# Kernel tuning notes

Measured on AMD Instinct MI355X. Metric: run time of the kernel, lower is better.

The kernel has to match this reference:

```python
import jax, jax.numpy as jnp
import numpy as np

N_NODES = 100_000
N_EDGES = 3_200_000
HIDDEN = 16


def setup_inputs() -> dict:
    key = jax.random.key(0)
    k1, k2, k3, k4 = jax.random.split(key, 4)
    x = jax.random.normal(k1, (N_NODES, 3), dtype=jnp.float32)
    edge_index = jax.random.randint(k2, (2, N_EDGES), 0, N_NODES, dtype=jnp.int32)
    # Glorot-style init for the two GCN layers (PyG GCNConv: lin weight + bias)
    W1 = jax.random.normal(k3, (3, HIDDEN), dtype=jnp.float32) * (1.0 / np.sqrt(3.0))
    b1 = jnp.zeros((HIDDEN,), dtype=jnp.float32)
    W2 = jax.random.normal(k4, (HIDDEN, 1), dtype=jnp.float32) * (1.0 / np.sqrt(HIDDEN))
    b2 = jnp.zeros((1,), dtype=jnp.float32)
    return {"x": x, "edge_index": edge_index, "W1": W1, "b1": b1, "W2": W2, "b2": b2}


def reference(x, edge_index, W1, b1, W2, b2):
    n = x.shape[0]  # static under jit
    # GCNConv default: add self-loops, symmetric degree normalization
    self_loop = jnp.arange(n, dtype=edge_index.dtype)
    src = jnp.concatenate([edge_index[0], self_loop])
    dst = jnp.concatenate([edge_index[1], self_loop])
    deg = jax.ops.segment_sum(jnp.ones_like(src, dtype=x.dtype), dst, num_segments=n)
    inv_sqrt_deg = jnp.where(deg > 0, jax.lax.rsqrt(jnp.maximum(deg, 1.0)), 0.0)
    norm = inv_sqrt_deg[src] * inv_sqrt_deg[dst]  # [E+N]

    def gcn_conv(h, W, b):
        h = h @ W  # linear transform first (cheaper: small out dim)
        msg = norm[:, None] * h[src]  # gather + scale
        return jax.ops.segment_sum(msg, dst, num_segments=n) + b  # scatter-add

    h = jax.nn.relu(gcn_conv(x, W1, b1))
    out = gcn_conv(h, W2, b2)
    return out.squeeze(-1)  # [N]
```

## Files before the change

kernel.cpp:

```cpp
#include <hip/hip_runtime.h>

#define HIDDEN 16
#define FB 128
#define FB_SHIFT 7
#define NBK_MAX 4096
#define FCHUNK 4096
#define FTH 512
#define STH 512
#define NXCD 8
#define CB 1024
#define CB_SHIFT 10
#define NCB_MAX 512
#define CHUNK 4096
#define SPL 8
#define BT 1024

__device__ __forceinline__ int xcd_chunk(int bid, int nwg) {
    if (nwg < NXCD) return bid;
    int q = nwg / NXCD, r = nwg % NXCD;
    int x = bid % NXCD, k = bid / NXCD;
    return (x < r ? x * (q + 1) : r * (q + 1) + (x - r) * q) + k;
}


__global__ __launch_bounds__(FTH) void
k_histf(const int* __restrict__ dst, int e, int nbk, int nchunk,
        unsigned int* __restrict__ hcT) {
    __shared__ unsigned int h[NBK_MAX];
    for (int i = threadIdx.x; i < nbk; i += FTH) h[i] = 0u;
    __syncthreads();
    int c = xcd_chunk(blockIdx.x, nchunk);
    int start = c * FCHUNK;
    int end = min(start + FCHUNK, e);
    if (end - start == FCHUNK) {
        int i = start + threadIdx.x;
#pragma unroll
        for (int k = 0; k < FCHUNK / FTH; k++, i += FTH)
            atomicAdd(&h[((unsigned)dst[i]) >> FB_SHIFT], 1u);
    } else {
        for (int i = start + threadIdx.x; i < end; i += FTH)
            atomicAdd(&h[((unsigned)dst[i]) >> FB_SHIFT], 1u);
    }
    __syncthreads();
    for (int j = threadIdx.x; j < nbk; j += FTH)
        hcT[(size_t)j * nchunk + c] = h[j];
}

__global__ void k_scanf(unsigned int* __restrict__ hcT,
                        unsigned int* __restrict__ cntc, int nchunk) {
    __shared__ unsigned int ps[256];
    __shared__ unsigned int carry;
    int b = blockIdx.x, t = threadIdx.x;
    if (t == 0) carry = 0u;
    __syncthreads();
    size_t row = (size_t)b * nchunk;
    for (int t0 = 0; t0 < nchunk; t0 += 1024) {
        int i0 = t0 + t * 4;
        unsigned v0 = 0, v1 = 0, v2 = 0, v3 = 0;
        if (i0 + 3 < nchunk) {
            v0 = hcT[row + i0];     v1 = hcT[row + i0 + 1];
            v2 = hcT[row + i0 + 2]; v3 = hcT[row + i0 + 3];
        } else {
            if (i0     < nchunk) v0 = hcT[row + i0];
            if (i0 + 1 < nchunk) v1 = hcT[row + i0 + 1];
            if (i0 + 2 < nchunk) v2 = hcT[row + i0 + 2];
            if (i0 + 3 < nchunk) v3 = hcT[row + i0 + 3];
        }
        unsigned s1v = v0 + v1, s2v = s1v + v2, s3v = s2v + v3;
        ps[t] = s3v;
        __syncthreads();
        for (int off = 1; off < 256; off <<= 1) {
            unsigned u = (t >= off) ? ps[t - off] : 0u;
            __syncthreads();
            ps[t] += u;
            __syncthreads();
        }
        unsigned base = carry + ps[t] - s3v;
        if (i0     < nchunk) hcT[row + i0]     = base;
        if (i0 + 1 < nchunk) hcT[row + i0 + 1] = base + v0;
        if (i0 + 2 < nchunk) hcT[row + i0 + 2] = base + s1v;
        if (i0 + 3 < nchunk) hcT[row + i0 + 3] = base + s2v;
        __syncthreads();
        if (t == 255) carry += ps[255];
        __syncthreads();
    }
    if (t == 0) cntc[b] = carry;
}

__global__ __launch_bounds__(1024) void
k_scanb(const unsigned int* __restrict__ cntc, int nbk,
        unsigned int* __restrict__ basec,
        unsigned int* __restrict__ rowptr, int n, unsigned int e) {
    __shared__ unsigned int tsum[1024];
    int t = threadIdx.x;
    int K = (nbk + 1023) / 1024;
    unsigned int s = 0;
    for (int k = 0; k < K; k++) {
        int i = t * K + k;
        if (i < nbk) s += cntc[i];
    }
    tsum[t] = s;
    __syncthreads();
    for (int off = 1; off < 1024; off <<= 1) {
        unsigned int v = (t >= off) ? tsum[t - off] : 0u;
        __syncthreads();
        tsum[t] += v;
        __syncthreads();
    }
    unsigned int run = (t == 0) ? 0u : tsum[t - 1];
    for (int k = 0; k < K; k++) {
        int i = t * K + k;
        if (i < nbk) { basec[i] = run; run += cntc[i]; }
    }
    if (t == 1023) basec[nbk] = tsum[1023];
    if (t == 0) rowptr[n] = e;
}

__global__ __launch_bounds__(FTH) void
k_fillf(const int* __restrict__ src, const int* __restrict__ dst,
        int e, int nbk, int nchunk,
        const unsigned int* __restrict__ basec,
        const unsigned int* __restrict__ hcT,
        unsigned int* __restrict__ tmp) {
    __shared__ unsigned int h[NBK_MAX];
    __shared__ unsigned int lb[NBK_MAX];
    int c = xcd_chunk(blockIdx.x, nchunk);
    for (int j = threadIdx.x; j < nbk; j += FTH) {
        lb[j] = basec[j] + hcT[(size_t)j * nchunk + c];
        h[j] = 0u;
    }
    __syncthreads();
    int start = c * FCHUNK;
    int end = min(start + FCHUNK, e);
    if (end - start == FCHUNK) {
        int i = start + threadIdx.x;
#pragma unroll
        for (int k = 0; k < FCHUNK / FTH; k++, i += FTH) {
            unsigned int d = (unsigned)dst[i];
            unsigned int s = (unsigned)src[i];
            unsigned int b = d >> FB_SHIFT;
            unsigned int r = atomicAdd(&h[b], 1u);
            tmp[lb[b] + r] = (s << FB_SHIFT) | (d & (FB - 1u));
        }
    } else {
        for (int i = start + threadIdx.x; i < end; i += FTH) {
            unsigned int d = (unsigned)dst[i];
            unsigned int s = (unsigned)src[i];
            unsigned int b = d >> FB_SHIFT;
            unsigned int r = atomicAdd(&h[b], 1u);
            tmp[lb[b] + r] = (s << FB_SHIFT) | (d & (FB - 1u));
        }
    }
}

__global__ __launch_bounds__(STH) void
k_sortN(const unsigned int* __restrict__ tmp,
        const unsigned int* __restrict__ basec,
        const float* __restrict__ x,
        unsigned int* __restrict__ rowptr, unsigned int* __restrict__ tmp2,
        float4* __restrict__ xs4, int n) {
    __shared__ unsigned int cnt[FB];
    __shared__ unsigned int sc[FB];
    __shared__ unsigned int cur[FB];
    int t = threadIdx.x, b = blockIdx.x;
    unsigned int s = basec[b], endp = basec[b + 1];
    if (t < FB) cnt[t] = 0u;
    __syncthreads();
    for (unsigned int i = s + t; i < endp; i += STH)
        atomicAdd(&cnt[tmp[i] & (FB - 1u)], 1u);
    __syncthreads();
    if (t < FB) sc[t] = cnt[t];
    __syncthreads();
    for (int off = 1; off < FB; off <<= 1) {
        unsigned int v = (t < FB && t >= off) ? sc[t - off] : 0u;
        __syncthreads();
        if (t < FB && t >= off) sc[t] += v;
        __syncthreads();
    }
    if (t < FB) {
        unsigned int excl = sc[t] - cnt[t];
        cur[t] = s + excl;
        int node = (b << FB_SHIFT) + t;
        if (node < n) {
            rowptr[node] = s + excl;
            float iv = rsqrtf((float)(1u + cnt[t]));
            xs4[node] = make_float4(x[3 * node] * iv, x[3 * node + 1] * iv,
                                    x[3 * node + 2] * iv, iv);
        }
    }
    __syncthreads();
    for (unsigned int i = s + t; i < endp; i += STH) {
        unsigned int rec = tmp[i];
        unsigned int r = atomicAdd(&cur[rec & (FB - 1u)], 1u);
        tmp2[r] = rec >> FB_SHIFT;
    }
}

__global__ void k_s1(const unsigned int* __restrict__ rowptr,
                     const unsigned int* __restrict__ tmp2,
                     const float4* __restrict__ xs4,
                     const float* __restrict__ W1, const float* __restrict__ b1,
                     const float* __restrict__ W2, const float* __restrict__ b2,
                     float* __restrict__ t2s, float* __restrict__ out, int n) {
    int gid = blockIdx.x * blockDim.x + threadIdx.x;
    int i = gid >> 2, q = gid & 3;
    bool valid = (i < n);
    unsigned int s = 0, epos = 0;
    if (valid) { s = rowptr[i]; epos = rowptr[i + 1]; }
    float v0 = 0.f, v1 = 0.f, v2 = 0.f;
    unsigned int j = s + q;
    for (; j + 12 < epos; j += 16) {
        unsigned a0 = tmp2[j], a1 = tmp2[j + 4], a2 = tmp2[j + 8], a3 = tmp2[j + 12];
        float4 p0 = xs4[a0], p1 = xs4[a1], p2 = xs4[a2], p3 = xs4[a3];
        v0 += (p0.x + p1.x) + (p2.x + p3.x);
        v1 += (p0.y + p1.y) + (p2.y + p3.y);
        v2 += (p0.z + p1.z) + (p2.z + p3.z);
    }
    for (; j < epos; j += 4) {
        float4 p = xs4[tmp2[j]];
        v0 += p.x; v1 += p.y; v2 += p.z;
    }
    v0 += __shfl_xor(v0, 1); v0 += __shfl_xor(v0, 2);
    v1 += __shfl_xor(v1, 1); v1 += __shfl_xor(v1, 2);
    v2 += __shfl_xor(v2, 1); v2 += __shfl_xor(v2, 2);
    if (valid && q == 0) {
        float4 me = xs4[i];
        float iv = me.w;
        v0 = (v0 + me.x) * iv;
        v1 = (v1 + me.y) * iv;
        v2 = (v2 + me.z) * iv;
        float acc = 0.f;
#pragma unroll
        for (int k = 0; k < HIDDEN; k++) {
            float hh = fmaxf(fmaf(v0, W1[k], fmaf(v1, W1[HIDDEN + k],
                            fmaf(v2, W1[2 * HIDDEN + k], b1[k]))), 0.f);
            acc += hh * W2[k];
        }
        t2s[i] = acc * iv;
        out[i] = b2[0] + acc * iv * iv;
    }
}

__global__ void k_s2(const unsigned int* __restrict__ rowptr,
                     const unsigned int* __restrict__ tmp2,
                     const float* __restrict__ t2s, const float4* __restrict__ xs4,
                     float* __restrict__ out, int n) {
    int gid = blockIdx.x * blockDim.x + threadIdx.x;
    int i = gid >> 2, q = gid & 3;
    bool valid = (i < n);
    unsigned int s = 0, epos = 0;
    if (valid) { s = rowptr[i]; epos = rowptr[i + 1]; }
    float v = 0.f;
    unsigned int j = s + q;
    for (; j + 12 < epos; j += 16) {
        unsigned a0 = tmp2[j], a1 = tmp2[j + 4], a2 = tmp2[j + 8], a3 = tmp2[j + 12];
        v += (t2s[a0] + t2s[a1]) + (t2s[a2] + t2s[a3]);
    }
    for (; j < epos; j += 4) v += t2s[tmp2[j]];
    v += __shfl_xor(v, 1); v += __shfl_xor(v, 2);
    if (valid && q == 0) out[i] += v * xs4[i].w;
}


__global__ void k_zero(unsigned int* a, int na) {
    int i = blockIdx.x * blockDim.x + threadIdx.x;
    if (i < na) a[i] = 0u;
}
__global__ void k_hist_c(const int* __restrict__ dst, int e, int ncb, int nchunk,
                         unsigned int* __restrict__ cntc,
                         unsigned int* __restrict__ hcT) {
    __shared__ unsigned int h[NCB_MAX];
    for (int i = threadIdx.x; i < ncb; i += blockDim.x) h[i] = 0u;
    __syncthreads();
    int start = blockIdx.x * CHUNK;
    int end = min(start + CHUNK, e);
    for (int i = start + threadIdx.x; i < end; i += 256)
        atomicAdd(&h[((unsigned)dst[i]) >> CB_SHIFT], 1u);
    __syncthreads();
    for (int j = threadIdx.x; j < ncb; j += blockDim.x) {
        hcT[(size_t)j * nchunk + blockIdx.x] = h[j];
        if (h[j]) atomicAdd(&cntc[j], h[j]);
    }
}
__global__ void k_scan(const unsigned int* __restrict__ cnt, int nb,
                       unsigned int* __restrict__ base) {
    __shared__ unsigned int tsum[256];
    int t = threadIdx.x;
    int K = (nb + 255) / 256;
    unsigned int s = 0;
    for (int k = 0; k < K; k++) {
        int i = t * K + k;
        if (i < nb) s += cnt[i];
    }
    tsum[t] = s;
    __syncthreads();
    for (int off = 1; off < 256; off <<= 1) {
        unsigned int v = (t >= off) ? tsum[t - off] : 0u;
        __syncthreads();
        tsum[t] += v;
        __syncthreads();
    }
    unsigned int run = (t == 0) ? 0u : tsum[t - 1];
    for (int k = 0; k < K; k++) {
        int i = t * K + k;
        if (i < nb) { base[i] = run; run += cnt[i]; }
    }
}
__global__ void k_scanc(const unsigned int* __restrict__ hcT,
                        const unsigned int* __restrict__ basec,
                        unsigned int* __restrict__ lbasec, int nchunk) {
    __shared__ unsigned int ts[256];
    __shared__ unsigned int carry;
    int b = blockIdx.x, t = threadIdx.x;
    if (t == 0) carry = basec[b];
    __syncthreads();
    for (int t0 = 0; t0 < nchunk; t0 += 256) {
        int i = t0 + t;
        unsigned int v = (i < nchunk) ? hcT[(size_t)b * nchunk + i] : 0u;
        ts[t] = v;
        __syncthreads();
        for (int off = 1; off < 256; off <<= 1) {
            unsigned int u = (t >= off) ? ts[t - off] : 0u;
            __syncthreads();
            ts[t] += u;
            __syncthreads();
        }
        if (i < nchunk) lbasec[(size_t)b * nchunk + i] = carry + ts[t] - v;
        __syncthreads();
        if (t == 0) carry += ts[255];
        __syncthreads();
    }
}
__global__ void k_fill_c(const int* __restrict__ src, const int* __restrict__ dst,
                         int e, int ncb, int nchunk,
                         const unsigned int* __restrict__ lbasec,
                         unsigned int* __restrict__ tmp) {
    __shared__ unsigned int h[NCB_MAX];
    __shared__ unsigned int lb[NCB_MAX];
    for (int j = threadIdx.x; j < ncb; j += blockDim.x) {
        lb[j] = lbasec[(size_t)j * nchunk + blockIdx.x];
        h[j] = 0u;
    }
    __syncthreads();
    int start = blockIdx.x * CHUNK;
    int end = min(start + CHUNK, e);
    for (int i = start + threadIdx.x; i < end; i += 256) {
        unsigned int d = (unsigned)dst[i];
        unsigned int b = d >> CB_SHIFT;
        unsigned int r = atomicAdd(&h[b], 1u);
        tmp[lb[b] + r] = (((unsigned)src[i]) << CB_SHIFT) | (d & (CB - 1u));
    }
}
__global__ __launch_bounds__(BT) void
k_deg_split(const unsigned int* __restrict__ tmp, const unsigned int* __restrict__ basec,
            const unsigned int* __restrict__ cntc, unsigned int* __restrict__ deg, int n) {
    __shared__ unsigned int degl[CB];
    int t = threadIdx.x;
    degl[t] = 0u;
    __syncthreads();
    int b = blockIdx.x / SPL, sl = blockIdx.x % SPL;
    unsigned int s = basec[b], m = cntc[b];
    for (unsigned int i = sl * BT + t; i < m; i += SPL * BT)
        atomicAdd(&degl[tmp[s + i] & (CB - 1u)], 1u);
    __syncthreads();
    int node = b * CB + t;
    unsigned int c = degl[t];
    if (node < n && c) atomicAdd(&deg[node], c);
}
__global__ void k_inv_s(const unsigned int* __restrict__ deg, const float* __restrict__ x,
                        float4* __restrict__ xs4, int n) {
    int i = blockIdx.x * blockDim.x + threadIdx.x;
    if (i >= n) return;
    float iv = rsqrtf((float)(deg[i] + 1u));
    xs4[i] = make_float4(x[3 * i] * iv, x[3 * i + 1] * iv, x[3 * i + 2] * iv, iv);
}
__global__ __launch_bounds__(BT) void
k_s1_split(const unsigned int* __restrict__ tmp, const unsigned int* __restrict__ basec,
           const unsigned int* __restrict__ cntc, const float4* __restrict__ xs4,
           float* __restrict__ agg0, float* __restrict__ agg1, float* __restrict__ agg2, int n) {
    __shared__ float a0[CB], a1[CB], a2[CB];
    int t = threadIdx.x;
    a0[t] = 0.f; a1[t] = 0.f; a2[t] = 0.f;
    __syncthreads();
    int b = blockIdx.x / SPL, sl = blockIdx.x % SPL;
    unsigned int s = basec[b], m = cntc[b];
    for (unsigned int i = sl * BT + t; i < m; i += SPL * BT) {
        unsigned rec = tmp[s + i];
        float4 v = xs4[rec >> CB_SHIFT];
        unsigned dl = rec & (CB - 1u);
        atomicAdd(&a0[dl], v.x); atomicAdd(&a1[dl], v.y); atomicAdd(&a2[dl], v.z);
    }
    __syncthreads();
    int node = b * CB + t;
    if (node < n) {
        if (a0[t] != 0.f) atomicAdd(&agg0[node], a0[t]);
        if (a1[t] != 0.f) atomicAdd(&agg1[node], a1[t]);
        if (a2[t] != 0.f) atomicAdd(&agg2[node], a2[t]);
    }
}
__global__ void k_epi_s(const float* __restrict__ agg0, const float* __restrict__ agg1,
                        const float* __restrict__ agg2, const float4* __restrict__ xs4,
                        const float* __restrict__ W1, const float* __restrict__ b1,
                        const float* __restrict__ W2, const float* __restrict__ b2,
                        float* __restrict__ t2s, float* __restrict__ out, int n) {
    int i = blockIdx.x * blockDim.x + threadIdx.x;
    if (i >= n) return;
    float4 xv = xs4[i];
    float iv = xv.w;
    float v0 = iv * (agg0[i] + xv.x), v1 = iv * (agg1[i] + xv.y), v2 = iv * (agg2[i] + xv.z);
    float acc = 0.f;
#pragma unroll
    for (int j = 0; j < HIDDEN; j++) {
        float h = fmaxf(fmaf(v0, W1[j], fmaf(v1, W1[HIDDEN + j],
                       fmaf(v2, W1[2 * HIDDEN + j], b1[j]))), 0.f);
        acc += h * W2[j];
    }
    t2s[i] = acc * iv;
    out[i] = b2[0] + acc * iv * iv;
}
__global__ __launch_bounds__(BT) void
k_s2_split(const unsigned int* __restrict__ tmp, const unsigned int* __restrict__ basec,
           const unsigned int* __restrict__ cntc, const float* __restrict__ t2s,
           const float4* __restrict__ xs4, float* __restrict__ out, int n) {
    __shared__ float o[CB];
    int t = threadIdx.x;
    o[t] = 0.f;
    __syncthreads();
    int b = blockIdx.x / SPL, sl = blockIdx.x % SPL;
    unsigned int s = basec[b], m = cntc[b];
    for (unsigned int i = sl * BT + t; i < m; i += SPL * BT) {
        unsigned rec = tmp[s + i];
        atomicAdd(&o[rec & (CB - 1u)], t2s[rec >> CB_SHIFT]);
    }
    __syncthreads();
    int node = b * CB + t;
    if (node < n && o[t] != 0.f) atomicAdd(&out[node], o[t] * xs4[node].w);
}


extern "C" void kernel_launch(void* const* d_in, const int* in_sizes, int n_in,
                              void* d_out, int out_size, void* d_ws, size_t ws_size,
                              hipStream_t stream) {
    const float* x  = (const float*)d_in[0];
    const int*   ei = (const int*)d_in[1];
    const float* W1 = (const float*)d_in[2];
    const float* b1 = (const float*)d_in[3];
    const float* W2 = (const float*)d_in[4];
    const float* b2 = (const float*)d_in[5];
    float* out = (float*)d_out;

    int n = in_sizes[0] / 3;
    int e = in_sizes[1] / 2;
    const int* src = ei;
    const int* dst = ei + e;
    const int B = 256;

    int nbk = (n + FB - 1) / FB;
    int nchunkf = (e + FCHUNK - 1) / FCHUNK;
    int gridN4 = (4 * n + B - 1) / B;

    size_t needf = (size_t)n * 16 + (size_t)n * 4 + (size_t)(n + 1) * 4
                 + (size_t)(2 * nbk + 1) * 4 + (size_t)nbk * nchunkf * 4
                 + (size_t)e * 8 + 64;

    if (nbk <= NBK_MAX && n < (1 << 25) && ws_size >= needf) {
        float4* xs4 = (float4*)d_ws;
        float* t2s = (float*)(xs4 + n);
        unsigned int* rowptr = (unsigned int*)(t2s + n);
        unsigned int* cntc   = rowptr + (n + 1);
        unsigned int* basec  = cntc + nbk;
        unsigned int* hcT    = basec + nbk + 1;
        unsigned int* tmp    = hcT + (size_t)nbk * nchunkf;
        unsigned int* tmp2   = tmp + e;

        k_histf<<<nchunkf, FTH, 0, stream>>>(dst, e, nbk, nchunkf, hcT);
        k_scanf<<<nbk, 256, 0, stream>>>(hcT, cntc, nchunkf);
        k_scanb<<<1, 1024, 0, stream>>>(cntc, nbk, basec, rowptr, n, (unsigned)e);
        k_fillf<<<nchunkf, FTH, 0, stream>>>(src, dst, e, nbk, nchunkf, basec, hcT, tmp);
        k_sortN<<<nbk, STH, 0, stream>>>(tmp, basec, x, rowptr, tmp2, xs4, n);
        k_s1<<<gridN4, B, 0, stream>>>(rowptr, tmp2, xs4, W1, b1, W2, b2, t2s, out, n);
        k_s2<<<gridN4, B, 0, stream>>>(rowptr, tmp2, t2s, xs4, out, n);
    } else {
        int ncb = (n + CB - 1) / CB;
        int gridE = (e + CHUNK - 1) / CHUNK;
        int gridN = (n + B - 1) / B;
        float4* xs4 = (float4*)d_ws;
        float* agg0 = (float*)(xs4 + n);
        float* agg1 = agg0 + n;
        float* agg2 = agg1 + n;
        unsigned int* deg = (unsigned int*)(agg2 + n);
        float* t2s = (float*)(deg + n);
        unsigned int* cntc   = (unsigned int*)(t2s + n);
        unsigned int* basec  = cntc + ncb;
        unsigned int* hcT    = basec + ncb;
        unsigned int* lbasec = hcT + (size_t)ncb * gridE;
        unsigned int* tmp    = lbasec + (size_t)ncb * gridE;

        k_zero<<<(4 * n + ncb + B - 1) / B, B, 0, stream>>>((unsigned int*)agg0, 4 * n);
        k_zero<<<(ncb + B - 1) / B, B, 0, stream>>>(cntc, ncb);
        k_hist_c<<<gridE, B, 0, stream>>>(dst, e, ncb, gridE, cntc, hcT);
        k_scan<<<1, B, 0, stream>>>(cntc, ncb, basec);
        k_scanc<<<ncb, B, 0, stream>>>(hcT, basec, lbasec, gridE);
        k_fill_c<<<gridE, B, 0, stream>>>(src, dst, e, ncb, gridE, lbasec, tmp);
        k_deg_split<<<ncb * SPL, BT, 0, stream>>>(tmp, basec, cntc, deg, n);
        k_inv_s<<<gridN, B, 0, stream>>>(deg, x, xs4, n);
        k_s1_split<<<ncb * SPL, BT, 0, stream>>>(tmp, basec, cntc, xs4, agg0, agg1, agg2, n);
        k_epi_s<<<gridN, B, 0, stream>>>(agg0, agg1, agg2, xs4, W1, b1, W2, b2, t2s, out, n);
        k_s2_split<<<ncb * SPL, BT, 0, stream>>>(tmp, basec, cntc, t2s, xs4, out, n);
    }
}
```

Baseline: 171.5 us.

## Fuse per-bucket sort with layer-1 aggregation and compute degrees via global atomics

Degrees are now counted with global atomics during the histogram pass. xs4 is built in the scan kernel, so the local sort no longer needs its own counting pass. The bucket sort and the first GCN layer are fused into one kernel: the bucket is sorted into LDS (capped at 5120 edges) and layer-1 aggregation reads neighbour ids from LDS, with a global fallback when the bucket is larger. This removes one launch and a re-read of tmp2 and rowptr. The cost is 3.2M extra global atomics in the histogram pass, one extra zeroing launch, and sort blocks with a large LDS footprint.

```diff
diff --git a/kernel.cpp b/kernel.cpp
--- a/kernel.cpp
+++ b/kernel.cpp
@@ -6,7 +6,7 @@
 #define NBK_MAX 4096
 #define FCHUNK 4096
 #define FTH 512
-#define STH 512
+#define SCAP 5120
 #define NXCD 8
 #define CB 1024
 #define CB_SHIFT 10
@@ -23,9 +23,14 @@
 }
 
 
+__global__ void k_zero(unsigned int* a, int na) {
+    int i = blockIdx.x * blockDim.x + threadIdx.x;
+    if (i < na) a[i] = 0u;
+}
+
 __global__ __launch_bounds__(FTH) void
 k_histf(const int* __restrict__ dst, int e, int nbk, int nchunk,
-        unsigned int* __restrict__ hcT) {
+        unsigned int* __restrict__ hcT, unsigned int* __restrict__ deg) {
     __shared__ unsigned int h[NBK_MAX];
     for (int i = threadIdx.x; i < nbk; i += FTH) h[i] = 0u;
     __syncthreads();
@@ -35,11 +40,17 @@
     if (end - start == FCHUNK) {
         int i = start + threadIdx.x;
 #pragma unroll
-        for (int k = 0; k < FCHUNK / FTH; k++, i += FTH)
-            atomicAdd(&h[((unsigned)dst[i]) >> FB_SHIFT], 1u);
+        for (int k = 0; k < FCHUNK / FTH; k++, i += FTH) {
+            unsigned int d = (unsigned)dst[i];
+            atomicAdd(&h[d >> FB_SHIFT], 1u);
+            atomicAdd(&deg[d], 1u);
+        }
     } else {
-        for (int i = start + threadIdx.x; i < end; i += FTH)
-            atomicAdd(&h[((unsigned)dst[i]) >> FB_SHIFT], 1u);
+        for (int i = start + threadIdx.x; i < end; i += FTH) {
+            unsigned int d = (unsigned)dst[i];
+            atomicAdd(&h[d >> FB_SHIFT], 1u);
+            atomicAdd(&deg[d], 1u);
+        }
     }
     __syncthreads();
     for (int j = threadIdx.x; j < nbk; j += FTH)
@@ -47,7 +58,10 @@
 }
 
 __global__ void k_scanf(unsigned int* __restrict__ hcT,
-                        unsigned int* __restrict__ cntc, int nchunk) {
+                        unsigned int* __restrict__ cntc, int nchunk,
+                        const unsigned int* __restrict__ deg,
+                        const float* __restrict__ x,
+                        float4* __restrict__ xs4, int n) {
     __shared__ unsigned int ps[256];
     __shared__ unsigned int carry;
     int b = blockIdx.x, t = threadIdx.x;
@@ -85,6 +99,14 @@
         __syncthreads();
     }
     if (t == 0) cntc[b] = carry;
+    if (t < FB) {
+        int node = (b << FB_SHIFT) + t;
+        if (node < n) {
+            float iv = rsqrtf((float)(1u + deg[node]));
+            xs4[node] = make_float4(x[3 * node] * iv, x[3 * node + 1] * iv,
+                                    x[3 * node + 2] * iv, iv);
+        }
+    }
 }
 
 __global__ __launch_bounds__(1024) void
@@ -153,23 +175,26 @@
     }
 }
 
-__global__ __launch_bounds__(STH) void
-k_sortN(const unsigned int* __restrict__ tmp,
-        const unsigned int* __restrict__ basec,
-        const float* __restrict__ x,
-        unsigned int* __restrict__ rowptr, unsigned int* __restrict__ tmp2,
-        float4* __restrict__ xs4, int n) {
-    __shared__ unsigned int cnt[FB];
+__global__ __launch_bounds__(FTH) void
+k_sortS1(const unsigned int* __restrict__ tmp,
+         const unsigned int* __restrict__ basec,
+         const unsigned int* __restrict__ deg,
+         const float4* __restrict__ xs4,
+         const float* __restrict__ W1, const float* __restrict__ b1,
+         const float* __restrict__ W2, const float* __restrict__ b2,
+         unsigned int* __restrict__ rowptr, unsigned int* __restrict__ tmp2,
+         float* __restrict__ t2s, float* __restrict__ out, int n) {
+    __shared__ unsigned int lsort[SCAP];
     __shared__ unsigned int sc[FB];
+    __shared__ unsigned int cnl[FB];
     __shared__ unsigned int cur[FB];
     int t = threadIdx.x, b = blockIdx.x;
-    unsigned int s = basec[b], endp = basec[b + 1];
-    if (t < FB) cnt[t] = 0u;
-    __syncthreads();
-    for (unsigned int i = s + t; i < endp; i += STH)
-        atomicAdd(&cnt[tmp[i] & (FB - 1u)], 1u);
-    __syncthreads();
-    if (t < FB) sc[t] = cnt[t];
+    unsigned int s = basec[b], endp = basec[b + 1], m = endp - s;
+    if (t < FB) {
+        int node = (b << FB_SHIFT) + t;
+        unsigned int c = (node < n) ? deg[node] : 0u;
+        cnl[t] = c; sc[t] = c;
+    }
     __syncthreads();
     for (int off = 1; off < FB; off <<= 1) {
         unsigned int v = (t < FB && t >= off) ? sc[t - off] : 0u;
@@ -178,53 +203,51 @@
         __syncthreads();
     }
     if (t < FB) {
-        unsigned int excl = sc[t] - cnt[t];
-        cur[t] = s + excl;
+        unsigned int excl = sc[t] - cnl[t];
+        cur[t] = excl;
         int node = (b << FB_SHIFT) + t;
-        if (node < n) {
-            rowptr[node] = s + excl;
-            float iv = rsqrtf((float)(1u + cnt[t]));
-            xs4[node] = make_float4(x[3 * node] * iv, x[3 * node + 1] * iv,
-                                    x[3 * node + 2] * iv, iv);
-        }
-    }
-    __syncthreads();
-    for (unsigned int i = s + t; i < endp; i += STH) {
-        unsigned int rec = tmp[i];
-        unsigned int r = atomicAdd(&cur[rec & (FB - 1u)], 1u);
-        tmp2[r] = rec >> FB_SHIFT;
-    }
-}
-
-__global__ void k_s1(const unsigned int* __restrict__ rowptr,
-                     const unsigned int* __restrict__ tmp2,
-                     const float4* __restrict__ xs4,
-                     const float* __restrict__ W1, const float* __restrict__ b1,
-                     const float* __restrict__ W2, const float* __restrict__ b2,
-                     float* __restrict__ t2s, float* __restrict__ out, int n) {
-    int gid = blockIdx.x * blockDim.x + threadIdx.x;
-    int i = gid >> 2, q = gid & 3;
-    bool valid = (i < n);
-    unsigned int s = 0, epos = 0;
-    if (valid) { s = rowptr[i]; epos = rowptr[i + 1]; }
+        if (node < n) rowptr[node] = s + excl;
+    }
+    __syncthreads();
+    bool fits = (m <= SCAP);
+    if (fits) {
+        for (unsigned int i = s + t; i < endp; i += FTH) {
+            unsigned int rec = tmp[i];
+            unsigned int r = atomicAdd(&cur[rec & (FB - 1u)], 1u);
+            lsort[r] = rec >> FB_SHIFT;
+        }
+        __syncthreads();
+        for (unsigned int k = t; k < m; k += FTH)
+            tmp2[s + k] = lsort[k];
+    } else {
+        for (unsigned int i = s + t; i < endp; i += FTH) {
+            unsigned int rec = tmp[i];
+            unsigned int r = atomicAdd(&cur[rec & (FB - 1u)], 1u);
+            tmp2[s + r] = rec >> FB_SHIFT;
+        }
+        __syncthreads();
+    }
+    int nl = t >> 2, q = t & 3;
+    int node = (b << FB_SHIFT) + nl;
+    unsigned int en = sc[nl];
+    unsigned int st = en - cnl[nl];
     float v0 = 0.f, v1 = 0.f, v2 = 0.f;
-    unsigned int j = s + q;
-    for (; j + 12 < epos; j += 16) {
-        unsigned a0 = tmp2[j], a1 = tmp2[j + 4], a2 = tmp2[j + 8], a3 = tmp2[j + 12];
-        float4 p0 = xs4[a0], p1 = xs4[a1], p2 = xs4[a2], p3 = xs4[a3];
-        v0 += (p0.x + p1.x) + (p2.x + p3.x);
-        v1 += (p0.y + p1.y) + (p2.y + p3.y);
-        v2 += (p0.z + p1.z) + (p2.z + p3.z);
-    }
-    for (; j < epos; j += 4) {
-        float4 p = xs4[tmp2[j]];
-        v0 += p.x; v1 += p.y; v2 += p.z;
+    if (fits) {
+        for (unsigned int k = st + q; k < en; k += 4) {
+            float4 p = xs4[lsort[k]];
+            v0 += p.x; v1 += p.y; v2 += p.z;
+        }
+    } else {
+        for (unsigned int k = st + q; k < en; k += 4) {
+            float4 p = xs4[tmp2[s + k]];
+            v0 += p.x; v1 += p.y; v2 += p.z;
+        }
     }
     v0 += __shfl_xor(v0, 1); v0 += __shfl_xor(v0, 2);
     v1 += __shfl_xor(v1, 1); v1 += __shfl_xor(v1, 2);
     v2 += __shfl_xor(v2, 1); v2 += __shfl_xor(v2, 2);
-    if (valid && q == 0) {
-        float4 me = xs4[i];
+    if (q == 0 && node < n) {
+        float4 me = xs4[node];
         float iv = me.w;
         v0 = (v0 + me.x) * iv;
         v1 = (v1 + me.y) * iv;
@@ -236,8 +259,8 @@
                             fmaf(v2, W1[2 * HIDDEN + k], b1[k]))), 0.f);
             acc += hh * W2[k];
         }
-        t2s[i] = acc * iv;
-        out[i] = b2[0] + acc * iv * iv;
+        t2s[node] = acc * iv;
+        out[node] = b2[0] + acc * iv * iv;
     }
 }
 
@@ -262,10 +285,6 @@
 }
 
 
-__global__ void k_zero(unsigned int* a, int na) {
-    int i = blockIdx.x * blockDim.x + threadIdx.x;
-    if (i < na) a[i] = 0u;
-}
 __global__ void k_hist_c(const int* __restrict__ dst, int e, int ncb, int nchunk,
                          unsigned int* __restrict__ cntc,
                          unsigned int* __restrict__ hcT) {
@@ -459,7 +478,7 @@
     int nchunkf = (e + FCHUNK - 1) / FCHUNK;
     int gridN4 = (4 * n + B - 1) / B;
 
-    size_t needf = (size_t)n * 16 + (size_t)n * 4 + (size_t)(n + 1) * 4
+    size_t needf = (size_t)n * 16 + (size_t)n * 4 + (size_t)(n + 1) * 4 + (size_t)n * 4
                  + (size_t)(2 * nbk + 1) * 4 + (size_t)nbk * nchunkf * 4
                  + (size_t)e * 8 + 64;
 
@@ -467,18 +486,20 @@
         float4* xs4 = (float4*)d_ws;
         float* t2s = (float*)(xs4 + n);
         unsigned int* rowptr = (unsigned int*)(t2s + n);
-        unsigned int* cntc   = rowptr + (n + 1);
+        unsigned int* deg    = rowptr + (n + 1);
+        unsigned int* cntc   = deg + n;
         unsigned int* basec  = cntc + nbk;
         unsigned int* hcT    = basec + nbk + 1;
         unsigned int* tmp    = hcT + (size_t)nbk * nchunkf;
         unsigned int* tmp2   = tmp + e;
 
-        k_histf<<<nchunkf, FTH, 0, stream>>>(dst, e, nbk, nchunkf, hcT);
-        k_scanf<<<nbk, 256, 0, stream>>>(hcT, cntc, nchunkf);
+        k_zero<<<(n + 1023) / 1024, 1024, 0, stream>>>(deg, n);
+        k_histf<<<nchunkf, FTH, 0, stream>>>(dst, e, nbk, nchunkf, hcT, deg);
+        k_scanf<<<nbk, 256, 0, stream>>>(hcT, cntc, nchunkf, deg, x, xs4, n);
         k_scanb<<<1, 1024, 0, stream>>>(cntc, nbk, basec, rowptr, n, (unsigned)e);
         k_fillf<<<nchunkf, FTH, 0, stream>>>(src, dst, e, nbk, nchunkf, basec, hcT, tmp);
-        k_sortN<<<nbk, STH, 0, stream>>>(tmp, basec, x, rowptr, tmp2, xs4, n);
-        k_s1<<<gridN4, B, 0, stream>>>(rowptr, tmp2, xs4, W1, b1, W2, b2, t2s, out, n);
+        k_sortS1<<<nbk, FTH, 0, stream>>>(tmp, basec, deg, xs4, W1, b1, W2, b2,
+                                          rowptr, tmp2, t2s, out, n);
         k_s2<<<gridN4, B, 0, stream>>>(rowptr, tmp2, t2s, xs4, out, n);
     } else {
         int ncb = (n + CB - 1) / CB;
```

Measured after the change: 287.0 us. 67.4% more time.
